# Kernel tuning notes

Hardware: AMD Instinct MI355X
Metric: run time of the kernel (lower is better)

Reference implementation:

```python
import jax, jax.numpy as jnp
import numpy as np

B, S, K, H = 8192, 512, 8, 512  # batch, size_half, n_segments, hidden
EPS = 1e-6


def setup_inputs() -> dict:
    key = jax.random.key(0)
    k0, k1, k2, k3 = jax.random.split(key, 4)
    x_input = jax.random.uniform(k0, (B, 2 * S), dtype=jnp.float32)  # in [0,1)
    log_density = jax.random.normal(k1, (B, 1), dtype=jnp.float32)
    W1 = jax.random.normal(k2, (S, H), dtype=jnp.float32) / np.sqrt(S).astype(np.float32)
    b1 = jnp.zeros((H,), jnp.float32)
    W2 = jax.random.normal(k3, (H, S * (2 * K + 1)), dtype=jnp.float32) / np.sqrt(H).astype(np.float32)
    b2 = jnp.zeros((S * (2 * K + 1),), jnp.float32)
    return {"x_input": x_input, "log_density": log_density,
            "W1": W1, "b1": b1, "W2": W2, "b2": b2}


def reference(x_input, log_density, W1, b1, W2, b2):
    # even_sites=True: passive half a = first S cols, transformed half b = last S
    x_a = x_input[:, :S]
    x_b = x_input[:, S:]

    # NeuralNetwork: Linear -> tanh -> Linear -> tanh (final_activation == activation)
    hid = jnp.tanh((x_a - 0.5) @ W1 + b1)
    net = jnp.tanh(hid @ W2 + b2).reshape(-1, S, 2 * K + 1)  # [B,S,2K+1]
    h_raw, w_raw = net[..., :K + 1], net[..., K + 1:]

    w_norm = jax.nn.softmax(w_raw, axis=2)                       # [B,S,K]
    eh = jnp.exp(h_raw)                                          # [B,S,K+1]
    h_norm = eh / jnp.sum(0.5 * w_norm * (eh[..., :-1] + eh[..., 1:]),
                          axis=2, keepdims=True)

    b = x_a.shape[0]
    x_knots = jnp.concatenate(
        [jnp.full((b, S, 1), -EPS, x_a.dtype), jnp.cumsum(w_norm, axis=2)], axis=2)  # [B,S,K+1]
    pdf_area = 0.5 * w_norm * (h_norm[..., :-1] + h_norm[..., 1:])
    phi_knots = jnp.concatenate(
        [jnp.zeros((b, S, 1), x_a.dtype), jnp.cumsum(pdf_area, axis=2)], axis=2)     # [B,S,K+1]

    # searchsorted(left) - 1 == (# knots strictly below x) - 1
    k_ind = jnp.clip(jnp.sum(x_knots < x_b[..., None], axis=2) - 1, 0, K - 1)[..., None]

    w_k = jnp.take_along_axis(w_norm, k_ind, axis=2)
    h_k = jnp.take_along_axis(h_norm, k_ind, axis=2)
    h_kp1 = jnp.take_along_axis(h_norm, k_ind + 1, axis=2)
    x_km1 = jnp.take_along_axis(x_knots, k_ind, axis=2)
    phi_km1 = jnp.take_along_axis(phi_knots, k_ind, axis=2)

    alpha = (x_b[..., None] - x_km1) / w_k
    phi_b = (phi_km1 + alpha * h_k * w_k
             + 0.5 * alpha ** 2 * (h_kp1 - h_k) * w_k)[..., 0]    # [B,S]

    phi_out = jnp.concatenate([x_a, phi_b], axis=1)               # [B,2S]
    new_log_density = log_density - jnp.sum(
        jnp.log(h_k + alpha * (h_kp1 - h_k)), axis=1)             # [B,1]
    return phi_out, new_log_density
```

## Files before the change

kernel.cpp:

```cpp
#include <hip/hip_runtime.h>
#include <stdint.h>
#include <math.h>

#define BROWS 8192
#define SDIM  512
#define HDIM  512
#define NCOL  8704
#define EPSK  1e-6f
#define LOG2E  1.442695041f
#define TWOL2E 2.885390082f
#define LN2    0.6931471806f

typedef __attribute__((ext_vector_type(8))) short bf16x8;
typedef __attribute__((ext_vector_type(4))) short bf16x4;
typedef __attribute__((ext_vector_type(4))) float f32x4;

__device__ __forceinline__ unsigned short f2bf(float f) {
    unsigned u = __float_as_uint(f);
    u += 0x7fffu + ((u >> 16) & 1u);
    return (unsigned short)(u >> 16);
}
__device__ __forceinline__ unsigned short f2bf_fast(float f) {
    return (unsigned short)((__float_as_uint(f) + 0x8000u) >> 16);
}
__device__ __forceinline__ float bf2f(unsigned short s) {
    return __uint_as_float(((unsigned)s) << 16);
}
#define EXP2F(x) __builtin_amdgcn_exp2f(x)
#define LOG2F(x) __builtin_amdgcn_logf(x)
#define RCPF(x)  __builtin_amdgcn_rcpf(x)

__device__ __forceinline__ float ftanh(float x) {
    float e = EXP2F(TWOL2E * x);
    return (e - 1.f) * RCPF(e + 1.f);
}
__device__ __forceinline__ float ftanh_l2e(float acc, float bias2L) {
    float e = EXP2F(fmaf(acc, TWOL2E, bias2L));
    return fmaf(e, LOG2E, -LOG2E) * RCPF(e + 1.f);
}

#define GLD16(g, l)                                                         \
    __builtin_amdgcn_global_load_lds(                                       \
        (const __attribute__((address_space(1))) void*)(g),                 \
        (__attribute__((address_space(3))) void*)(l), 16, 0, 0)

__global__ __launch_bounds__(256) void prep_k(
    const float* __restrict__ W2, unsigned short* __restrict__ W2p,
    const float* __restrict__ W1, unsigned short* __restrict__ W1T,
    const float* __restrict__ logd, float* __restrict__ out)
{
    __shared__ float tile[32 * 33];
    const int t = threadIdx.x;
    if (blockIdx.x < 544) {
        const int ct = blockIdx.x;
        const int colbase = ct * 16;
        const int colblk = ct / 17;
        const int chunk  = ct - colblk * 17;
        const int k32 = t >> 3;
        const int c2  = (t & 7) * 2;
        const int r   = t >> 4;
        const int e2  = (t & 15) * 2;
        for (int kk = 0; kk < 16; ++kk) {
            float2 v = *(const float2*)&W2[(size_t)(kk * 32 + k32) * NCOL + colbase + c2];
            __syncthreads();
            tile[k32 * 17 + c2 + 0] = v.x;
            tile[k32 * 17 + c2 + 1] = v.y;
            __syncthreads();
            const size_t off = (((size_t)colblk * 16 + kk) * 17 + chunk) * 512;
            ushort2 o;
            o.x = f2bf(tile[(e2 + 0) * 17 + r]);
            o.y = f2bf(tile[(e2 + 1) * 17 + r]);
            *(ushort2*)&W2p[off + (size_t)r * 32 + e2] = o;
        }
    } else if (blockIdx.x < 800) {
        const int bt = blockIdx.x - 544;
        const int cb = (bt & 15) * 32;
        const int rb = (bt >> 4) * 32;
        const int ty = t >> 3, tx = (t & 7) * 4;
        float4 v = *(const float4*)&W1[(size_t)(rb + ty) * HDIM + cb + tx];
        tile[ty * 33 + tx + 0] = v.x;
        tile[ty * 33 + tx + 1] = v.y;
        tile[ty * 33 + tx + 2] = v.z;
        tile[ty * 33 + tx + 3] = v.w;
        __syncthreads();
        const int oy = t >> 3, ox = (t & 7) * 4;
        bf16x4 o;
        o[0] = (short)f2bf(tile[(ox + 0) * 33 + oy]);
        o[1] = (short)f2bf(tile[(ox + 1) * 33 + oy]);
        o[2] = (short)f2bf(tile[(ox + 2) * 33 + oy]);
        o[3] = (short)f2bf(tile[(ox + 3) * 33 + oy]);
        *(bf16x4*)&W1T[(size_t)(cb + oy) * SDIM + rb + ox] = o;
    } else {
        const int b = (blockIdx.x - 800) * 256 + t;
        out[(size_t)BROWS * (2 * SDIM) + b] = logd[b];
    }
}

__global__ __launch_bounds__(256) void gemm1_mfma(
    const float* __restrict__ x,
    const unsigned short* __restrict__ W1T,
    const float* __restrict__ b1,
    unsigned short* __restrict__ hid,
    float* __restrict__ out)
{
    __shared__ short As[64 * 32];
    __shared__ short Bs[128 * 32];
    const int bm   = blockIdx.y * 64;
    const int bn   = blockIdx.x * 128;
    const int tid  = threadIdx.x;
    const int lane = tid & 63;
    const int wave = tid >> 6;
    const int ln15 = lane & 15;
    const int quad = lane >> 4;
    const int wm   = (wave >> 1) * 32;
    const int wn   = (wave & 1) * 64;
    const int arow = tid >> 2, aseg = tid & 3;
    const int brow = lane >> 2, bsub = lane & 3;

    f32x4 acc[2][4];
#pragma unroll
    for (int i = 0; i < 2; i++)
#pragma unroll
        for (int j = 0; j < 4; j++) acc[i][j] = (f32x4){0.f, 0.f, 0.f, 0.f};

    for (int k0 = 0; k0 < SDIM; k0 += 32) {
        const float4* xq = (const float4*)&x[(size_t)(bm + arow) * (2 * SDIM) + k0 + aseg * 8];
        float4 f0 = xq[0], f1 = xq[1];
        if (blockIdx.x == 0) {
            float* op = &out[(size_t)(bm + arow) * (2 * SDIM) + k0 + aseg * 8];
            *(float4*)op = f0;
            *(float4*)(op + 4) = f1;
        }
        __syncthreads();
#pragma unroll
        for (int c = 0; c < 2; c++) {
            const int chunk = wave * 2 + c;
            GLD16(&W1T[(size_t)(bn + chunk * 16 + brow) * SDIM + k0 + bsub * 8],
                  &Bs[chunk * 512]);
        }
        bf16x8 v0;
        v0[0] = (short)f2bf_fast(f0.x - 0.5f); v0[1] = (short)f2bf_fast(f0.y - 0.5f);
        v0[2] = (short)f2bf_fast(f0.z - 0.5f); v0[3] = (short)f2bf_fast(f0.w - 0.5f);
        v0[4] = (short)f2bf_fast(f1.x - 0.5f); v0[5] = (short)f2bf_fast(f1.y - 0.5f);
        v0[6] = (short)f2bf_fast(f1.z - 0.5f); v0[7] = (short)f2bf_fast(f1.w - 0.5f);
        *(bf16x8*)&As[arow * 32 + aseg * 8] = v0;
        __syncthreads();

        bf16x8 af[2], bfr[4];
#pragma unroll
        for (int i = 0; i < 2; i++)
            af[i] = *(const bf16x8*)&As[(wm + i * 16 + ln15) * 32 + quad * 8];
#pragma unroll
        for (int j = 0; j < 4; j++)
            bfr[j] = *(const bf16x8*)&Bs[(wn + j * 16 + ln15) * 32 + quad * 8];
#pragma unroll
        for (int i = 0; i < 2; i++)
#pragma unroll
            for (int j = 0; j < 4; j++)
                acc[i][j] = __builtin_amdgcn_mfma_f32_16x16x32_bf16(af[i], bfr[j], acc[i][j], 0, 0, 0);
    }

#pragma unroll
    for (int j = 0; j < 4; j++) {
        const int col = bn + wn + j * 16 + ln15;
        const float bias = b1[col];
#pragma unroll
        for (int i = 0; i < 2; i++) {
#pragma unroll
            for (int r = 0; r < 4; r++) {
                const int row = bm + wm + i * 16 + quad * 4 + r;
                hid[(size_t)row * HDIM + col] = f2bf(ftanh(acc[i][j][r] + bias));
            }
        }
    }
}

__global__ __launch_bounds__(256, 3) void gemm2_spline_mfma(
    const unsigned short* __restrict__ hid,
    const unsigned short* __restrict__ W2p,
    const float* __restrict__ b2,
    const float* __restrict__ x,
    float* __restrict__ out)
{
    __shared__ short smem[2 * 10752];

    const int bm     = blockIdx.x * 64;
    const int colblk = blockIdx.y;
    const int tid  = threadIdx.x;
    const int lane = tid & 63;
    const int wave = tid >> 6;
    const int ln15 = lane & 15;
    const int quad = lane >> 4;
    const int brow = lane >> 2, bsub = lane & 3;
    const int jstart = wave * 4;
    const int jcount = (wave == 3) ? 5 : 4;
    const int bcol = colblk * 272;

    f32x4 acc[4][5];
#pragma unroll
    for (int i = 0; i < 4; i++)
#pragma unroll
        for (int j = 0; j < 5; j++) acc[i][j] = (f32x4){0.f, 0.f, 0.f, 0.f};

    const unsigned short* bbase =
        W2p + ((size_t)colblk * 16) * 17 * 512 + (size_t)lane * 8;
    const unsigned short* abase =
        &hid[(size_t)(bm + wave * 16 + brow) * HDIM + bsub * 8];

    auto issue = [&](int n, int p) {
        short* dst = smem + p * 10752;
        GLD16(abase + n * 32, &dst[wave * 512]);
        const unsigned short* bk = bbase + (size_t)n * (17 * 512);
        for (int c = 0; c < jcount; ++c) {
            const int chunk = jstart + c;
            GLD16(bk + (size_t)chunk * 512, &dst[2048 + chunk * 512]);
        }
    };

    issue(0, 0);
    for (int n = 0; n < 16; ++n) {
        __syncthreads();
        if (n < 15) issue(n + 1, (n + 1) & 1);
        const short* As = smem + (n & 1) * 10752;
        const short* Bs = As + 2048;

        bf16x8 af[4];
#pragma unroll
        for (int i = 0; i < 4; i++)
            af[i] = *(const bf16x8*)&As[(i * 16 + ln15) * 32 + quad * 8];

#define KSTEP(JC)                                                               \
        _Pragma("unroll") for (int j = 0; j < (JC); ++j) {                      \
            bf16x8 bfr = *(const bf16x8*)&Bs[((jstart + j) * 16 + ln15) * 32 + quad * 8]; \
            _Pragma("unroll") for (int i = 0; i < 4; ++i)                       \
                acc[i][j] = __builtin_amdgcn_mfma_f32_16x16x32_bf16(af[i], bfr, acc[i][j], 0, 0, 0); \
        }
        if (wave == 3) { KSTEP(5) } else { KSTEP(4) }
#undef KSTEP
    }

    const int sp = tid & 15;
    const int r0 = tid >> 4;
    const int sglob = colblk * 16 + sp;
    float xbv[4];
#pragma unroll
    for (int t = 0; t < 4; ++t)
        xbv[t] = x[(size_t)(bm + t * 16 + r0) * (2 * SDIM) + SDIM + sglob];

    __syncthreads();
#define EPI1(JC)                                                                \
    _Pragma("unroll") for (int j = 0; j < (JC); ++j) {                          \
        const int col_l = (jstart + j) * 16 + ln15;                             \
        const float bias2L = b2[bcol + col_l] * TWOL2E;                         \
        _Pragma("unroll") for (int i = 0; i < 4; ++i) {                         \
            bf16x4 o;                                                           \
            _Pragma("unroll") for (int r = 0; r < 4; ++r)                       \
                o[r] = (short)f2bf_fast(ftanh_l2e(acc[i][j][r], bias2L));       \
            *(bf16x4*)&smem[col_l * 68 + i * 16 + quad * 4] = o;                \
        }                                                                       \
    }
    if (wave == 3) { EPI1(5) } else { EPI1(4) }
#undef EPI1
    __syncthreads();

    for (int t = 0; t < 4; ++t) {
        const int row_l = t * 16 + r0;
        const int row = bm + row_l;
        const int cbase = sp * 17 * 68 + row_l;

        float s[17];
#pragma unroll
        for (int c = 0; c < 17; c++)
            s[c] = bf2f((unsigned short)smem[cbase + c * 68]);

        float eh[9], e[8];
#pragma unroll
        for (int j = 0; j < 9; j++) eh[j] = EXP2F(s[j]);
#pragma unroll
        for (int c = 0; c < 8; c++) e[c]  = EXP2F(s[9 + c]);

        float cum_e[8], cum_u[8];
        cum_e[0] = e[0];
        cum_u[0] = e[0] * (eh[0] + eh[1]);
#pragma unroll
        for (int c = 1; c < 8; c++) {
            cum_e[c] = cum_e[c - 1] + e[c];
            cum_u[c] = fmaf(e[c], eh[c] + eh[c + 1], cum_u[c - 1]);
        }
        const float se = cum_e[7];
        const float su = cum_u[7];
        const float thr = xbv[t] * se;

        float selE = e[0], selEH = eh[0], selEH1 = eh[1];
        float selCE = -EPSK * se, selCU = 0.f;
#pragma unroll
        for (int c = 1; c < 8; c++) {
            const bool tt = (cum_e[c - 1] < thr);
            selE   = tt ? e[c]         : selE;
            selEH  = tt ? eh[c]        : selEH;
            selEH1 = tt ? eh[c + 1]    : selEH1;
            selCE  = tt ? cum_e[c - 1] : selCE;
            selCU  = tt ? cum_u[c - 1] : selCU;
        }

        const float alpha = (thr - selCE) * RCPF(selE);
        const float dlt   = selEH1 - selEH;
        const float su_inv = RCPF(su);
        float p = fmaf(2.f * alpha, selE * selEH, selCU);
        p = fmaf(alpha * alpha, selE * dlt, p);
        out[(size_t)row * (2 * SDIM) + SDIM + sglob] = p * su_inv;

        const float g = fmaf(alpha, dlt, selEH) * (2.f * se * su_inv);
        float lg = LOG2F(g);
        lg += __shfl_xor(lg, 1);
        lg += __shfl_xor(lg, 2);
        lg += __shfl_xor(lg, 4);
        lg += __shfl_xor(lg, 8);
        if (sp == 0)
            atomicAdd(&out[(size_t)BROWS * (2 * SDIM) + row], -lg * LN2);
    }
}

extern "C" void kernel_launch(void* const* d_in, const int* in_sizes, int n_in,
                              void* d_out, int out_size, void* d_ws, size_t ws_size,
                              hipStream_t stream) {
    const float* x    = (const float*)d_in[0];
    const float* logd = (const float*)d_in[1];
    const float* W1   = (const float*)d_in[2];
    const float* b1   = (const float*)d_in[3];
    const float* W2   = (const float*)d_in[4];
    const float* b2   = (const float*)d_in[5];
    float* out = (float*)d_out;

    char* ws = (char*)d_ws;
    unsigned short* W1T = (unsigned short*)(ws + 32768);
    unsigned short* W2p = (unsigned short*)(ws + 557056);
    unsigned short* hid = (unsigned short*)(ws + 9469952);

    prep_k<<<832, 256, 0, stream>>>(W2, W2p, W1, W1T, logd, out);
    gemm1_mfma<<<dim3(4, 128), 256, 0, stream>>>(x, W1T, b1, hid, out);
    gemm2_spline_mfma<<<dim3(128, 32), 256, 0, stream>>>(hid, W2p, b2, x, out);
}
```

Before: 232.6 us.

## Double-buffer gemm1 with async LDS loads, swizzle LDS, split prep work

gemm1 now streams raw fp32 x tiles and W1T tiles into double-buffered LDS through global_load_lds and converts to bf16 when reading from LDS, replacing the synchronous register load and store per k-step. LDS layouts in both GEMMs are XOR-swizzled to cut bank conflicts, and gemm1 blocks are remapped so each XCD gets contiguous row tiles. The prep kernel splits the W2 repack across four times as many blocks and takes over the x_a passthrough copy from gemm1. Costs are more LDS per gemm1 block from the fp32 double buffer and a larger prep launch.

```diff
diff --git a/kernel.cpp b/kernel.cpp
--- a/kernel.cpp
+++ b/kernel.cpp
@@ -47,12 +47,15 @@
 __global__ __launch_bounds__(256) void prep_k(
     const float* __restrict__ W2, unsigned short* __restrict__ W2p,
     const float* __restrict__ W1, unsigned short* __restrict__ W1T,
-    const float* __restrict__ logd, float* __restrict__ out)
+    const float* __restrict__ logd, float* __restrict__ out,
+    const float* __restrict__ x)
 {
     __shared__ float tile[32 * 33];
-    const int t = threadIdx.x;
-    if (blockIdx.x < 544) {
-        const int ct = blockIdx.x;
+    const int t   = threadIdx.x;
+    const int bid = blockIdx.x;
+    if (bid < 2176) {
+        const int ct = bid >> 2;
+        const int kq = bid & 3;
         const int colbase = ct * 16;
         const int colblk = ct / 17;
         const int chunk  = ct - colblk * 17;
@@ -60,7 +63,7 @@
         const int c2  = (t & 7) * 2;
         const int r   = t >> 4;
         const int e2  = (t & 15) * 2;
-        for (int kk = 0; kk < 16; ++kk) {
+        for (int kk = kq * 4; kk < kq * 4 + 4; ++kk) {
             float2 v = *(const float2*)&W2[(size_t)(kk * 32 + k32) * NCOL + colbase + c2];
             __syncthreads();
             tile[k32 * 17 + c2 + 0] = v.x;
@@ -72,8 +75,8 @@
             o.y = f2bf(tile[(e2 + 1) * 17 + r]);
             *(ushort2*)&W2p[off + (size_t)r * 32 + e2] = o;
         }
-    } else if (blockIdx.x < 800) {
-        const int bt = blockIdx.x - 544;
+    } else if (bid < 2432) {
+        const int bt = bid - 2176;
         const int cb = (bt & 15) * 32;
         const int rb = (bt >> 4) * 32;
         const int ty = t >> 3, tx = (t & 7) * 4;
@@ -90,8 +93,19 @@
         o[2] = (short)f2bf(tile[(ox + 2) * 33 + oy]);
         o[3] = (short)f2bf(tile[(ox + 3) * 33 + oy]);
         *(bf16x4*)&W1T[(size_t)(cb + oy) * SDIM + rb + ox] = o;
+    } else if (bid < 2688) {
+        const int bt = bid - 2432;
+        const float4* xi = (const float4*)x;
+        float4* oo = (float4*)out;
+        const int base = bt * 4096 + t;
+#pragma unroll
+        for (int k2 = 0; k2 < 16; ++k2) {
+            const int f = base + k2 * 256;
+            const int row = f >> 7, c4 = f & 127;
+            oo[(size_t)row * 256 + c4] = xi[(size_t)row * 256 + c4];
+        }
     } else {
-        const int b = (blockIdx.x - 800) * 256 + t;
+        const int b = (bid - 2688) * 256 + t;
         out[(size_t)BROWS * (2 * SDIM) + b] = logd[b];
     }
 }
@@ -100,13 +114,17 @@
     const float* __restrict__ x,
     const unsigned short* __restrict__ W1T,
     const float* __restrict__ b1,
-    unsigned short* __restrict__ hid,
-    float* __restrict__ out)
+    unsigned short* __restrict__ hid)
 {
-    __shared__ short As[64 * 32];
-    __shared__ short Bs[128 * 32];
-    const int bm   = blockIdx.y * 64;
-    const int bn   = blockIdx.x * 128;
+    __shared__ float Asf[2][64 * 32];
+    __shared__ short Bsb[2][128 * 32];
+
+    const int flat = blockIdx.y * 4 + blockIdx.x;
+    const int xcd  = flat & 7;
+    const int j8   = flat >> 3;
+    const int bn   = (j8 & 3) * 128;
+    const int bm   = (xcd * 16 + (j8 >> 2)) * 64;
+
     const int tid  = threadIdx.x;
     const int lane = tid & 63;
     const int wave = tid >> 6;
@@ -114,8 +132,12 @@
     const int quad = lane >> 4;
     const int wm   = (wave >> 1) * 32;
     const int wn   = (wave & 1) * 64;
-    const int arow = tid >> 2, aseg = tid & 3;
-    const int brow = lane >> 2, bsub = lane & 3;
+    const int brow = lane >> 2;
+    const int bsub_sw = (lane & 3) ^ ((lane >> 3) & 3);
+    const int arow8   = lane >> 3;
+    const int aslot_sw = (lane & 7) ^ (arow8 & 7);
+    const int qsw = (quad ^ ((ln15 >> 1) & 3)) * 8;
+    const int ag  = ln15 & 7;
 
     f32x4 acc[2][4];
 #pragma unroll
@@ -123,40 +145,49 @@
 #pragma unroll
         for (int j = 0; j < 4; j++) acc[i][j] = (f32x4){0.f, 0.f, 0.f, 0.f};
 
-    for (int k0 = 0; k0 < SDIM; k0 += 32) {
-        const float4* xq = (const float4*)&x[(size_t)(bm + arow) * (2 * SDIM) + k0 + aseg * 8];
-        float4 f0 = xq[0], f1 = xq[1];
-        if (blockIdx.x == 0) {
-            float* op = &out[(size_t)(bm + arow) * (2 * SDIM) + k0 + aseg * 8];
-            *(float4*)op = f0;
-            *(float4*)(op + 4) = f1;
-        }
+    const float* asrc = &x[(size_t)(bm + arow8) * (2 * SDIM) + aslot_sw * 4];
+    const unsigned short* bsrc = &W1T[(size_t)(bn + brow) * SDIM + bsub_sw * 8];
+
+    auto issue = [&](int n, int p) {
+#pragma unroll
+        for (int c = 0; c < 2; ++c) {
+            const int ca = wave * 2 + c;
+            GLD16(asrc + (size_t)ca * 8 * (2 * SDIM) + n * 32, &Asf[p][ca * 256]);
+        }
+#pragma unroll
+        for (int c = 0; c < 2; ++c) {
+            const int cb = wave * 2 + c;
+            GLD16(bsrc + (size_t)cb * 16 * SDIM + n * 32, &Bsb[p][cb * 512]);
+        }
+    };
+
+    issue(0, 0);
+    for (int n = 0; n < 16; ++n) {
         __syncthreads();
-#pragma unroll
-        for (int c = 0; c < 2; c++) {
-            const int chunk = wave * 2 + c;
-            GLD16(&W1T[(size_t)(bn + chunk * 16 + brow) * SDIM + k0 + bsub * 8],
-                  &Bs[chunk * 512]);
-        }
-        bf16x8 v0;
-        v0[0] = (short)f2bf_fast(f0.x - 0.5f); v0[1] = (short)f2bf_fast(f0.y - 0.5f);
-        v0[2] = (short)f2bf_fast(f0.z - 0.5f); v0[3] = (short)f2bf_fast(f0.w - 0.5f);
-        v0[4] = (short)f2bf_fast(f1.x - 0.5f); v0[5] = (short)f2bf_fast(f1.y - 0.5f);
-        v0[6] = (short)f2bf_fast(f1.z - 0.5f); v0[7] = (short)f2bf_fast(f1.w - 0.5f);
-        *(bf16x8*)&As[arow * 32 + aseg * 8] = v0;
-        __syncthreads();
+        if (n < 15) issue(n + 1, (n + 1) & 1);
+        const float* As = Asf[n & 1];
+        const short* Bs = Bsb[n & 1];
 
         bf16x8 af[2], bfr[4];
 #pragma unroll
-        for (int i = 0; i < 2; i++)
-            af[i] = *(const bf16x8*)&As[(wm + i * 16 + ln15) * 32 + quad * 8];
-#pragma unroll
-        for (int j = 0; j < 4; j++)
-            bfr[j] = *(const bf16x8*)&Bs[(wn + j * 16 + ln15) * 32 + quad * 8];
-#pragma unroll
-        for (int i = 0; i < 2; i++)
-#pragma unroll
-            for (int j = 0; j < 4; j++)
+        for (int i = 0; i < 2; ++i) {
+            const int r = wm + i * 16 + ln15;
+            f32x4 a0 = *(const f32x4*)&As[r * 32 + ((2 * quad + 0) ^ ag) * 4];
+            f32x4 a1 = *(const f32x4*)&As[r * 32 + ((2 * quad + 1) ^ ag) * 4];
+            bf16x8 v;
+            v[0] = (short)f2bf_fast(a0[0] - 0.5f); v[1] = (short)f2bf_fast(a0[1] - 0.5f);
+            v[2] = (short)f2bf_fast(a0[2] - 0.5f); v[3] = (short)f2bf_fast(a0[3] - 0.5f);
+            v[4] = (short)f2bf_fast(a1[0] - 0.5f); v[5] = (short)f2bf_fast(a1[1] - 0.5f);
+            v[6] = (short)f2bf_fast(a1[2] - 0.5f); v[7] = (short)f2bf_fast(a1[3] - 0.5f);
+            af[i] = v;
+        }
+#pragma unroll
+        for (int j = 0; j < 4; ++j)
+            bfr[j] = *(const bf16x8*)&Bs[(wn + j * 16 + ln15) * 32 + qsw];
+#pragma unroll
+        for (int i = 0; i < 2; ++i)
+#pragma unroll
+            for (int j = 0; j < 4; ++j)
                 acc[i][j] = __builtin_amdgcn_mfma_f32_16x16x32_bf16(af[i], bfr[j], acc[i][j], 0, 0, 0);
     }
 
@@ -191,7 +222,9 @@
     const int wave = tid >> 6;
     const int ln15 = lane & 15;
     const int quad = lane >> 4;
-    const int brow = lane >> 2, bsub = lane & 3;
+    const int brow = lane >> 2;
+    const int bsub_sw = (lane & 3) ^ ((lane >> 3) & 3);
+    const int qsw = (quad ^ ((ln15 >> 1) & 3)) * 8;
     const int jstart = wave * 4;
     const int jcount = (wave == 3) ? 5 : 4;
     const int bcol = colblk * 272;
@@ -203,9 +236,9 @@
         for (int j = 0; j < 5; j++) acc[i][j] = (f32x4){0.f, 0.f, 0.f, 0.f};
 
     const unsigned short* bbase =
-        W2p + ((size_t)colblk * 16) * 17 * 512 + (size_t)lane * 8;
+        W2p + ((size_t)colblk * 16) * 17 * 512 + (size_t)(lane >> 2) * 32 + (size_t)bsub_sw * 8;
     const unsigned short* abase =
-        &hid[(size_t)(bm + wave * 16 + brow) * HDIM + bsub * 8];
+        &hid[(size_t)(bm + wave * 16 + brow) * HDIM + bsub_sw * 8];
 
     auto issue = [&](int n, int p) {
         short* dst = smem + p * 10752;
@@ -227,11 +260,11 @@
         bf16x8 af[4];
 #pragma unroll
         for (int i = 0; i < 4; i++)
-            af[i] = *(const bf16x8*)&As[(i * 16 + ln15) * 32 + quad * 8];
+            af[i] = *(const bf16x8*)&As[(i * 16 + ln15) * 32 + qsw];
 
 #define KSTEP(JC)                                                               \
         _Pragma("unroll") for (int j = 0; j < (JC); ++j) {                      \
-            bf16x8 bfr = *(const bf16x8*)&Bs[((jstart + j) * 16 + ln15) * 32 + quad * 8]; \
+            bf16x8 bfr = *(const bf16x8*)&Bs[((jstart + j) * 16 + ln15) * 32 + qsw]; \
             _Pragma("unroll") for (int i = 0; i < 4; ++i)                       \
                 acc[i][j] = __builtin_amdgcn_mfma_f32_16x16x32_bf16(af[i], bfr, acc[i][j], 0, 0, 0); \
         }
@@ -337,7 +370,7 @@
     unsigned short* W2p = (unsigned short*)(ws + 557056);
     unsigned short* hid = (unsigned short*)(ws + 9469952);
 
-    prep_k<<<832, 256, 0, stream>>>(W2, W2p, W1, W1T, logd, out);
-    gemm1_mfma<<<dim3(4, 128), 256, 0, stream>>>(x, W1T, b1, hid, out);
+    prep_k<<<2720, 256, 0, stream>>>(W2, W2p, W1, W1T, logd, out, x);
+    gemm1_mfma<<<dim3(4, 128), 256, 0, stream>>>(x, W1T, b1, hid);
     gemm2_spline_mfma<<<dim3(128, 32), 256, 0, stream>>>(hid, W2p, b2, x, out);
 }
```

New measurement: 229.3 us. About the same (-1.4%).
